# Optimization experiments

Hardware: AMD Instinct MI355X
Metric: run time of the kernel (lower is better)

## Reference

```python
import jax, jax.numpy as jnp
import numpy as np

IMAGE = 224
PAD = 30            # max_pad_size
CROP = IMAGE - 2 * PAD  # 164
NCAM = 3
B, T = 16, 16


def setup_inputs() -> dict:
    key = jax.random.key(0)
    ks = jax.random.split(key, 12)
    x = jax.random.normal(ks[0], (B, 3, T, IMAGE, IMAGE), dtype=jnp.float32)
    cam_idx = jax.random.randint(ks[1], (B,), 0, NCAM, dtype=jnp.int32)
    # original uses np.random.randint(1, max_pad+1)
    off_right = jax.random.randint(ks[2], (B,), 1, PAD + 1, dtype=jnp.int32)
    off_down = jax.random.randint(ks[3], (B,), 1, PAD + 1, dtype=jnp.int32)
    # learned pad strips, stacked over the 3 cam views (ParameterDict order)
    pad_up_1 = jax.random.normal(ks[4], (NCAM, 3, 1, IMAGE), dtype=jnp.float32)
    pad_up_10 = jax.random.normal(ks[5], (NCAM, 3, 10, IMAGE), dtype=jnp.float32)
    pad_down_1 = jax.random.normal(ks[6], (NCAM, 3, 1, IMAGE), dtype=jnp.float32)
    pad_down_10 = jax.random.normal(ks[7], (NCAM, 3, 10, IMAGE), dtype=jnp.float32)
    pad_left_1 = jax.random.normal(ks[8], (NCAM, 3, CROP, 1), dtype=jnp.float32)
    pad_left_10 = jax.random.normal(ks[9], (NCAM, 3, CROP, 10), dtype=jnp.float32)
    pad_right_1 = jax.random.normal(ks[10], (NCAM, 3, CROP, 1), dtype=jnp.float32)
    pad_right_10 = jax.random.normal(ks[11], (NCAM, 3, CROP, 10), dtype=jnp.float32)
    return dict(x=x, pad_up_1=pad_up_1, pad_up_10=pad_up_10,
                pad_down_1=pad_down_1, pad_down_10=pad_down_10,
                pad_left_1=pad_left_1, pad_left_10=pad_left_10,
                pad_right_1=pad_right_1, pad_right_10=pad_right_10,
                cam_idx=cam_idx, off_right=off_right, off_down=off_down)


def _build_prompt(ci, orr, od,
                  pad_up_1, pad_up_10, pad_down_1, pad_down_10,
                  pad_left_1, pad_left_10, pad_right_1, pad_right_10):
    # per-sample prompt image [3, IMAGE, IMAGE]; fused gather version of the
    # per-strip torch.cat construction.
    pu1 = pad_up_1[ci, :, 0, :]        # [3, W]
    pu10 = pad_up_10[ci]               # [3, 10, W]
    pd1 = pad_down_1[ci, :, 0, :]      # [3, W]
    pd10 = pad_down_10[ci]             # [3, 10, W]
    pl1 = pad_left_1[ci, :, :, 0]      # [3, CROP]
    pl10 = pad_left_10[ci]             # [3, CROP, 10]
    pr1 = pad_right_1[ci, :, :, 0]     # [3, CROP]
    pr10 = pad_right_10[ci]            # [3, CROP, 10]

    off_l = 2 * PAD - orr
    off_u = 2 * PAD - od
    n10_l, n1_l = off_l // 10, off_l % 10
    n10_u, n1_u = off_u // 10, off_u % 10
    n1_r = orr % 10
    n1_d = od % 10

    h = jnp.arange(IMAGE)
    w = jnp.arange(IMAGE)
    hh = h[:, None]                    # [H,1]
    ww = w[None, :]                    # [1,W]

    # top band: n10_u copies of 10-strip then n1_u copies of 1-strip
    up = jnp.where(hh < n10_u * 10, pu10[:, h % 10, :], pu1[:, None, :])  # [3,H,W]
    # bottom band: n1_d copies of 1-strip then 10-strips
    hd = hh - (IMAGE - od)
    di = jnp.mod(hd - n1_d, 10)[:, 0]
    down = jnp.where(hd < n1_d, pd1[:, None, :], pd10[:, di, :])          # [3,H,W]

    r = jnp.clip(h - off_u, 0, CROP - 1)                                   # [H]
    left = jnp.where(ww < n10_l * 10,
                     pl10[:, r[:, None], (w % 10)[None, :]],
                     pl1[:, r, None])                                      # [3,H,W]
    wd = w - (IMAGE - orr)
    ri = jnp.mod(wd - n1_r, 10)
    right = jnp.where(wd[None, :] < n1_r,
                      pr1[:, r, None],
                      pr10[:, r[:, None], ri[None, :]])                    # [3,H,W]

    mid = jnp.where(ww < off_l, left,
                    jnp.where(ww >= IMAGE - orr, right, jnp.float32(0.0)))
    return jnp.where(hh < off_u, up,
                     jnp.where(hh >= IMAGE - od, down, mid))               # [3,H,W]


def reference(x, pad_up_1, pad_up_10, pad_down_1, pad_down_10,
              pad_left_1, pad_left_10, pad_right_1, pad_right_10,
              cam_idx, off_right, off_down):
    build = lambda ci, orr, od: _build_prompt(
        ci, orr, od, pad_up_1, pad_up_10, pad_down_1, pad_down_10,
        pad_left_1, pad_left_10, pad_right_1, pad_right_10)
    prompt = jax.vmap(build)(cam_idx, off_right, off_down)  # [B,3,H,W]
    return x + prompt[:, :, None, :, :]                     # [B,3,T,H,W]
```

## Files before the change

### kernel.cpp

```cpp
#include <hip/hip_runtime.h>

#define IMAGE 224
#define PAD   30
#define CROP  164
#define BATCH 16
#define TT    16
#define W4    56

__global__ __launch_bounds__(256) void prompt_add_kernel(
    const float* __restrict__ x,
    const float* __restrict__ pu1,  const float* __restrict__ pu10,
    const float* __restrict__ pd1,  const float* __restrict__ pd10,
    const float* __restrict__ pl1,  const float* __restrict__ pl10,
    const float* __restrict__ pr1,  const float* __restrict__ pr10,
    const int* __restrict__ cam_idx,
    const int* __restrict__ off_right,
    const int* __restrict__ off_down,
    float* __restrict__ out)
{
    const int idx = blockIdx.x * blockDim.x + threadIdx.x;
    const int total = BATCH * 3 * TT * IMAGE * W4;
    if (idx >= total) return;

    const int w4 = idx % W4;
    const int h  = (idx / W4) % IMAGE;
    const int c  = (idx / (W4 * IMAGE * TT)) % 3;
    const int b  =  idx / (W4 * IMAGE * TT * 3);

    const int ci    = cam_idx[b];
    const int orr   = off_right[b];
    const int od    = off_down[b];
    const int off_l = 2 * PAD - orr;
    const int off_u = 2 * PAD - od;
    const int n10_l = off_l / 10;
    const int n10_u = off_u / 10;
    const int n1_r  = orr % 10;
    const int n1_d  = od % 10;

    const int w0      = w4 * 4;
    const int base_cc = ci * 3 + c;

    float p[4];

    if (h < off_u) {
        const float* rowp = (h < n10_u * 10)
            ? (pu10 + (size_t)(base_cc * 10 + (h % 10)) * IMAGE)
            : (pu1  + (size_t)base_cc * IMAGE);
        #pragma unroll
        for (int j = 0; j < 4; ++j) p[j] = rowp[w0 + j];
    } else if (h >= IMAGE - od) {
        const int hd = h - (IMAGE - od);
        const float* rowp = (hd < n1_d)
            ? (pd1  + (size_t)base_cc * IMAGE)
            : (pd10 + (size_t)(base_cc * 10 + ((hd - n1_d) % 10)) * IMAGE);
        #pragma unroll
        for (int j = 0; j < 4; ++j) p[j] = rowp[w0 + j];
    } else {
        int r = h - off_u;
        r = r < 0 ? 0 : (r > CROP - 1 ? CROP - 1 : r);
        #pragma unroll
        for (int j = 0; j < 4; ++j) {
            const int w = w0 + j;
            float v;
            if (w < off_l) {
                v = (w < n10_l * 10)
                    ? pl10[((size_t)base_cc * CROP + r) * 10 + (w % 10)]
                    : pl1 [ (size_t)base_cc * CROP + r];
            } else if (w >= IMAGE - orr) {
                const int wd = w - (IMAGE - orr);
                v = (wd < n1_r)
                    ? pr1 [ (size_t)base_cc * CROP + r]
                    : pr10[((size_t)base_cc * CROP + r) * 10 + ((wd - n1_r) % 10)];
            } else {
                v = 0.0f;
            }
            p[j] = v;
        }
    }

    const size_t off = (size_t)idx * 4;
    const float4 xv = *reinterpret_cast<const float4*>(x + off);
    float4 ov;
    ov.x = xv.x + p[0];
    ov.y = xv.y + p[1];
    ov.z = xv.z + p[2];
    ov.w = xv.w + p[3];
    *reinterpret_cast<float4*>(out + off) = ov;
}

extern "C" void kernel_launch(void* const* d_in, const int* in_sizes, int n_in,
                              void* d_out, int out_size, void* d_ws, size_t ws_size,
                              hipStream_t stream) {
    const float* x    = (const float*)d_in[0];
    const float* pu1  = (const float*)d_in[1];
    const float* pu10 = (const float*)d_in[2];
    const float* pd1  = (const float*)d_in[3];
    const float* pd10 = (const float*)d_in[4];
    const float* pl1  = (const float*)d_in[5];
    const float* pl10 = (const float*)d_in[6];
    const float* pr1  = (const float*)d_in[7];
    const float* pr10 = (const float*)d_in[8];
    const int* cam_idx   = (const int*)d_in[9];
    const int* off_right = (const int*)d_in[10];
    const int* off_down  = (const int*)d_in[11];
    float* out = (float*)d_out;

    const int total  = BATCH * 3 * TT * IMAGE * W4;
    const int block  = 256;
    const int grid   = (total + block - 1) / block;

    prompt_add_kernel<<<grid, block, 0, stream>>>(
        x, pu1, pu10, pd1, pd10, pl1, pl10, pr1, pr10,
        cam_idx, off_right, off_down, out);
}
```

Measured before the change: 277.5 us.

## Compute prompt once per pixel and loop over time dimension with nontemporal IO

After: 274.3 us. No clear change (-1.2%).

```diff
diff --git a/kernel.cpp b/kernel.cpp
--- a/kernel.cpp
+++ b/kernel.cpp
@@ -6,6 +6,10 @@
 #define BATCH 16
 #define TT    16
 #define W4    56
+#define HW4   (IMAGE * W4)
+#define BLOCKS_PER_BC 49
+
+typedef float f32x4 __attribute__((ext_vector_type(4)));
 
 __global__ __launch_bounds__(256) void prompt_add_kernel(
     const float* __restrict__ x,
@@ -18,14 +22,12 @@
     const int* __restrict__ off_down,
     float* __restrict__ out)
 {
-    const int idx = blockIdx.x * blockDim.x + threadIdx.x;
-    const int total = BATCH * 3 * TT * IMAGE * W4;
-    if (idx >= total) return;
-
-    const int w4 = idx % W4;
-    const int h  = (idx / W4) % IMAGE;
-    const int c  = (idx / (W4 * IMAGE * TT)) % 3;
-    const int b  =  idx / (W4 * IMAGE * TT * 3);
+    const int bid = blockIdx.x;
+    const int b   = bid / (3 * BLOCKS_PER_BC);
+    const int c   = (bid / BLOCKS_PER_BC) % 3;
+    const int loc = (bid % BLOCKS_PER_BC) * 256 + threadIdx.x;
+    const int h   = loc / W4;
+    const int w4  = loc % W4;
 
     const int ci    = cam_idx[b];
     const int orr   = off_right[b];
@@ -40,24 +42,25 @@
     const int w0      = w4 * 4;
     const int base_cc = ci * 3 + c;
 
-    float p[4];
+    float p0, p1, p2, p3;
 
     if (h < off_u) {
         const float* rowp = (h < n10_u * 10)
             ? (pu10 + (size_t)(base_cc * 10 + (h % 10)) * IMAGE)
             : (pu1  + (size_t)base_cc * IMAGE);
-        #pragma unroll
-        for (int j = 0; j < 4; ++j) p[j] = rowp[w0 + j];
+        const float4 pv = *reinterpret_cast<const float4*>(rowp + w0);
+        p0 = pv.x; p1 = pv.y; p2 = pv.z; p3 = pv.w;
     } else if (h >= IMAGE - od) {
         const int hd = h - (IMAGE - od);
         const float* rowp = (hd < n1_d)
             ? (pd1  + (size_t)base_cc * IMAGE)
             : (pd10 + (size_t)(base_cc * 10 + ((hd - n1_d) % 10)) * IMAGE);
-        #pragma unroll
-        for (int j = 0; j < 4; ++j) p[j] = rowp[w0 + j];
+        const float4 pv = *reinterpret_cast<const float4*>(rowp + w0);
+        p0 = pv.x; p1 = pv.y; p2 = pv.z; p3 = pv.w;
     } else {
         int r = h - off_u;
         r = r < 0 ? 0 : (r > CROP - 1 ? CROP - 1 : r);
+        float p[4];
         #pragma unroll
         for (int j = 0; j < 4; ++j) {
             const int w = w0 + j;
@@ -76,16 +79,27 @@
             }
             p[j] = v;
         }
+        p0 = p[0]; p1 = p[1]; p2 = p[2]; p3 = p[3];
     }
 
-    const size_t off = (size_t)idx * 4;
-    const float4 xv = *reinterpret_cast<const float4*>(x + off);
-    float4 ov;
-    ov.x = xv.x + p[0];
-    ov.y = xv.y + p[1];
-    ov.z = xv.z + p[2];
-    ov.w = xv.w + p[3];
-    *reinterpret_cast<float4*>(out + off) = ov;
+    const size_t plane  = (size_t)IMAGE * IMAGE;
+    const size_t sbase  = ((size_t)(b * 3 + c) * TT) * plane
+                        + (size_t)h * IMAGE + w0;
+    const float* xp = x   + sbase;
+    float*       op = out + sbase;
+
+    #pragma unroll
+    for (int t = 0; t < TT; ++t) {
+        const f32x4 xv = __builtin_nontemporal_load(
+            reinterpret_cast<const f32x4*>(xp + (size_t)t * plane));
+        f32x4 ov;
+        ov.x = xv.x + p0;
+        ov.y = xv.y + p1;
+        ov.z = xv.z + p2;
+        ov.w = xv.w + p3;
+        __builtin_nontemporal_store(ov,
+            reinterpret_cast<f32x4*>(op + (size_t)t * plane));
+    }
 }
 
 extern "C" void kernel_launch(void* const* d_in, const int* in_sizes, int n_in,
@@ -105,9 +119,8 @@
     const int* off_down  = (const int*)d_in[11];
     float* out = (float*)d_out;
 
-    const int total  = BATCH * 3 * TT * IMAGE * W4;
-    const int block  = 256;
-    const int grid   = (total + block - 1) / block;
+    const int grid  = BATCH * 3 * BLOCKS_PER_BC;
+    const int block = 256;
 
     prompt_add_kernel<<<grid, block, 0, stream>>>(
         x, pu1, pu10, pd1, pd10, pl1, pl10, pr1, pr10,
```
